# Kernel tuning notes

Hardware: AMD Instinct MI355X
Metric: run time of the kernel (lower is better)

The kernel has to match this reference:

```python
import jax, jax.numpy as jnp
import numpy as np

NEG_SLOPE = 0.2
EPS = 1e-16

N_NODES = 100000
N_EDGES = 1600000
IN_CH = 128
HEADS = 4
OUT_CH = 32


def setup_inputs() -> dict:
    key = jax.random.key(0)
    k1, k2, k3, k4, k5 = jax.random.split(key, 5)
    x = jax.random.normal(k1, (N_NODES, IN_CH), dtype=jnp.float32)
    edge_index = jax.random.randint(k2, (2, N_EDGES), 0, N_NODES, dtype=jnp.int64)
    glorot = (6.0 / (IN_CH + HEADS * OUT_CH)) ** 0.5
    W_l = jax.random.uniform(k3, (IN_CH, HEADS * OUT_CH), jnp.float32, -glorot, glorot)
    W_r = jax.random.uniform(k4, (IN_CH, HEADS * OUT_CH), jnp.float32, -glorot, glorot)
    ga = (6.0 / (OUT_CH + 1)) ** 0.5
    att = jax.random.uniform(k5, (HEADS, OUT_CH), jnp.float32, -ga, ga)
    bias = jnp.zeros((HEADS * OUT_CH,), dtype=jnp.float32)
    return {"x": x, "edge_index": edge_index, "W_l": W_l, "W_r": W_r, "att": att, "bias": bias}


def reference(x, edge_index, W_l, W_r, att, bias):
    # GATv2Conv forward (PyG semantics, concat=True, add_self_loops=False)
    N = x.shape[0]
    H, C = att.shape
    src, dst = edge_index[0], edge_index[1]

    x_l = (x @ W_l).reshape(N, H, C)  # source transform
    x_r = (x @ W_r).reshape(N, H, C)  # target transform

    # per-edge attention logits: e_ij = att . leaky_relu(x_l[j] + x_r[i])
    h = x_l[src] + x_r[dst]                      # [E, H, C]
    e = jnp.einsum('ehc,hc->eh', jax.nn.leaky_relu(h, NEG_SLOPE), att)  # [E, H]

    # segment softmax over edges grouped by destination node
    m = jax.ops.segment_max(e, dst, num_segments=N)      # [N, H]
    e_exp = jnp.exp(e - m[dst])                          # [E, H]
    denom = jax.ops.segment_sum(e_exp, dst, num_segments=N)  # [N, H]
    alpha = e_exp / (denom[dst] + EPS)                   # [E, H]

    # attention-weighted message aggregation
    msg = x_l[src] * alpha[:, :, None]                   # [E, H, C]
    out = jax.ops.segment_sum(msg, dst, num_segments=N)  # [N, H, C]
    return out.reshape(N, H * C) + bias
```

## Files before the change

### kernel.cpp

```cpp
#include <hip/hip_runtime.h>
#include <hip/hip_bf16.h>
#include <cstdint>
#include <cstddef>


#define NEG_SLOPE 0.2f
#define EPS_F 1e-16f
#define NRANGE 8
#define NCHUNK 64
#define SORT_B 1024
#define MAX_RSZ 12512

typedef __attribute__((ext_vector_type(8))) short bf16x8;
typedef __attribute__((ext_vector_type(4))) float f32x4;

static __device__ __forceinline__ unsigned f2bf(float f) {
    unsigned u = __float_as_uint(f);
    return (u + 0x7fffu + ((u >> 16) & 1u)) >> 16;
}
static __device__ __forceinline__ float bf2f(unsigned h) {
    return __uint_as_float(h << 16);
}

__global__ __launch_bounds__(SORT_B) void histW_k(const int* __restrict__ dst, int E, int N,
                                                  int rsz, int chunk_e,
                                                  unsigned* __restrict__ g,
                                                  const float* __restrict__ Wl,
                                                  const float* __restrict__ Wr,
                                                  unsigned short* __restrict__ Wtl,
                                                  unsigned short* __restrict__ Wtr) {
    if (blockIdx.x == NRANGE * NCHUNK) {
        for (int mat = 0; mat < 2; ++mat) {
            const float* W = mat ? Wr : Wl;
            unsigned short* Wt = mat ? Wtr : Wtl;
            for (int i = 0; i < 16; ++i) {
                int idx = (int)threadIdx.x + i * SORT_B;
                int k = idx >> 7, n = idx & 127;
                Wt[n * 128 + k] = (unsigned short)f2bf(W[idx]);
            }
        }
        return;
    }
    __shared__ unsigned lcnt[MAX_RSZ];
    const int r = blockIdx.x & (NRANGE - 1);
    const int c = blockIdx.x >> 3;
    const unsigned r_lo = (unsigned)(r * rsz);
    const int e0 = c * chunk_e;
    const int e1 = min(e0 + chunk_e, E);

    for (int i = threadIdx.x; i < rsz; i += SORT_B) lcnt[i] = 0u;
    __syncthreads();
    for (int e = e0 + (int)threadIdx.x; e < e1; e += SORT_B) {
        unsigned dd = (unsigned)dst[e] - r_lo;
        if (dd < (unsigned)rsz) atomicAdd(&lcnt[dd], 1u);
    }
    __syncthreads();
    unsigned* gc = g + (size_t)c * N + r_lo;
    int lim = min(rsz, N - (int)r_lo);
    for (int i = threadIdx.x; i < lim; i += SORT_B) gc[i] = lcnt[i];
}

#define LROW 136
__global__ __launch_bounds__(256) void mfma_gemm_k(const float* __restrict__ A,
                                                   const unsigned short* __restrict__ Wtl,
                                                   const unsigned short* __restrict__ Wtr,
                                                   unsigned short* __restrict__ xl,
                                                   unsigned short* __restrict__ xr,
                                                   int nrows) {
    __shared__ unsigned short As[64 * LROW];
    __shared__ unsigned short Ws[128 * LROW];
    const int tid = threadIdx.x;
    const int wave = tid >> 6, lane = tid & 63;
    const int quad = lane >> 4, m16 = lane & 15;
    const int row0 = blockIdx.x * 64;

#pragma unroll
    for (int i = 0; i < 8; ++i) {
        int idx = tid + i * 256;
        int r = idx >> 5, c4 = idx & 31;
        int gr = row0 + r;
        gr = gr < nrows ? gr : nrows - 1;
        float4 v = *(const float4*)(A + (size_t)gr * 128 + c4 * 4);
        ushort4 b;
        b.x = (unsigned short)f2bf(v.x);
        b.y = (unsigned short)f2bf(v.y);
        b.z = (unsigned short)f2bf(v.z);
        b.w = (unsigned short)f2bf(v.w);
        *(ushort4*)(&As[r * LROW + c4 * 4]) = b;
    }
#pragma unroll
    for (int i = 0; i < 8; ++i) {
        int idx = tid + i * 256;
        int n = idx >> 4, kq = idx & 15;
        *(uint4*)(&Ws[n * LROW + kq * 8]) = *(const uint4*)(Wtl + n * 128 + kq * 8);
    }
    __syncthreads();

    bf16x8 af[4];
#pragma unroll
    for (int ks = 0; ks < 4; ++ks)
        af[ks] = *(const bf16x8*)(&As[(wave * 16 + m16) * LROW + ks * 32 + quad * 8]);

    f32x4 acc[8];
#pragma unroll
    for (int ct = 0; ct < 8; ++ct) acc[ct] = (f32x4){0.f, 0.f, 0.f, 0.f};
#pragma unroll
    for (int ct = 0; ct < 8; ++ct)
#pragma unroll
        for (int ks = 0; ks < 4; ++ks) {
            bf16x8 bf = *(const bf16x8*)(&Ws[(ct * 16 + m16) * LROW + ks * 32 + quad * 8]);
            acc[ct] = __builtin_amdgcn_mfma_f32_16x16x32_bf16(af[ks], bf, acc[ct], 0, 0, 0);
        }
#pragma unroll
    for (int ct = 0; ct < 8; ++ct)
#pragma unroll
        for (int r = 0; r < 4; ++r) {
            int grow = row0 + wave * 16 + quad * 4 + r;
            if (grow < nrows) xl[(size_t)grow * 128 + ct * 16 + m16] = (unsigned short)f2bf(acc[ct][r]);
        }

    __syncthreads();
#pragma unroll
    for (int i = 0; i < 8; ++i) {
        int idx = tid + i * 256;
        int n = idx >> 4, kq = idx & 15;
        *(uint4*)(&Ws[n * LROW + kq * 8]) = *(const uint4*)(Wtr + n * 128 + kq * 8);
    }
    __syncthreads();

#pragma unroll
    for (int ct = 0; ct < 8; ++ct) acc[ct] = (f32x4){0.f, 0.f, 0.f, 0.f};
#pragma unroll
    for (int ct = 0; ct < 8; ++ct)
#pragma unroll
        for (int ks = 0; ks < 4; ++ks) {
            bf16x8 bf = *(const bf16x8*)(&Ws[(ct * 16 + m16) * LROW + ks * 32 + quad * 8]);
            acc[ct] = __builtin_amdgcn_mfma_f32_16x16x32_bf16(af[ks], bf, acc[ct], 0, 0, 0);
        }
#pragma unroll
    for (int ct = 0; ct < 8; ++ct)
#pragma unroll
        for (int r = 0; r < 4; ++r) {
            int grow = row0 + wave * 16 + quad * 4 + r;
            if (grow < nrows) xr[(size_t)grow * 128 + ct * 16 + m16] = (unsigned short)f2bf(acc[ct][r]);
        }
}

__global__ __launch_bounds__(256) void colsum_k(const unsigned* __restrict__ g, int N,
                                                int* __restrict__ cnt) {
    int d = blockIdx.x * 256 + threadIdx.x;
    if (d >= N) return;
    unsigned s = 0;
#pragma unroll
    for (int c = 0; c < NCHUNK; ++c) s += g[(size_t)c * N + d];
    cnt[d] = (int)s;
}

#define SCAN_B 256
__global__ __launch_bounds__(SCAN_B) void scanA_k(const int* __restrict__ cnt, int n,
                                                  int* __restrict__ row_start,
                                                  int* __restrict__ bsum) {
    const int tid = threadIdx.x, lane = tid & 63, wid = tid >> 6;
    const int g = blockIdx.x * SCAN_B + tid;
    int v = (g < n) ? cnt[g] : 0;
    int inc = v;
#pragma unroll
    for (int d = 1; d < 64; d <<= 1) {
        int t = __shfl_up(inc, d);
        if (lane >= d) inc += t;
    }
    __shared__ int wsum[SCAN_B / 64];
    if (lane == 63) wsum[wid] = inc;
    __syncthreads();
    int add = 0;
    for (int w = 0; w < wid; ++w) add += wsum[w];
    inc += add;
    if (g < n) row_start[g] = inc - v;
    if (tid == SCAN_B - 1) bsum[blockIdx.x] = inc;
}

__global__ __launch_bounds__(512) void scanB_k(int* __restrict__ bsum, int nb) {
    const int tid = threadIdx.x, lane = tid & 63, wid = tid >> 6;
    int v = (tid < nb) ? bsum[tid] : 0;
    int inc = v;
#pragma unroll
    for (int d = 1; d < 64; d <<= 1) {
        int t = __shfl_up(inc, d);
        if (lane >= d) inc += t;
    }
    __shared__ int wsum[8];
    if (lane == 63) wsum[wid] = inc;
    __syncthreads();
    int add = 0;
    for (int w = 0; w < wid; ++w) add += wsum[w];
    inc += add;
    if (tid < nb) bsum[tid] = inc - v;
}

__global__ __launch_bounds__(SCAN_B) void scanC_k(int* __restrict__ row_start,
                                                  const int* __restrict__ bsum,
                                                  int n, int E,
                                                  int* __restrict__ src_sorted) {
    const int g = blockIdx.x * SCAN_B + threadIdx.x;
    if (g < n) row_start[g] += bsum[blockIdx.x];
    if (g == 0) row_start[n] = E;
    if (blockIdx.x == 0 && threadIdx.x < 8) src_sorted[E + threadIdx.x] = 0;
}

__global__ __launch_bounds__(256) void cbase_k(const unsigned* __restrict__ g,
                                               const int* __restrict__ row_start, int N,
                                               unsigned* __restrict__ base) {
    int d = blockIdx.x * 256 + threadIdx.x;
    if (d >= N) return;
    unsigned run = (unsigned)row_start[d];
#pragma unroll
    for (int c = 0; c < NCHUNK; ++c) {
        base[(size_t)c * N + d] = run;
        run += g[(size_t)c * N + d];
    }
}

__global__ __launch_bounds__(SORT_B) void scat_k(const int* __restrict__ src,
                                                 const int* __restrict__ dst, int E, int N,
                                                 int rsz, int chunk_e,
                                                 const unsigned* __restrict__ base,
                                                 int* __restrict__ src_sorted) {
    __shared__ unsigned lcur[MAX_RSZ];
    const int r = blockIdx.x & (NRANGE - 1);
    const int c = blockIdx.x >> 3;
    const unsigned r_lo = (unsigned)(r * rsz);
    const int e0 = c * chunk_e;
    const int e1 = min(e0 + chunk_e, E);

    const unsigned* bc = base + (size_t)c * N + r_lo;
    int lim = min(rsz, N - (int)r_lo);
    for (int i = threadIdx.x; i < lim; i += SORT_B) lcur[i] = bc[i];
    __syncthreads();

    for (int e = e0 + (int)threadIdx.x; e < e1; e += SORT_B) {
        unsigned dd = (unsigned)dst[e] - r_lo;
        if (dd < (unsigned)rsz) {
            unsigned pos = atomicAdd(&lcur[dd], 1u);
            src_sorted[pos] = src[e];
        }
    }
}

__global__ __launch_bounds__(256) void agg_k(const unsigned* __restrict__ xlb,
                                             const unsigned* __restrict__ xrb,
                                             const float* __restrict__ att,
                                             const float* __restrict__ bias,
                                             const int* __restrict__ row_start,
                                             const int* __restrict__ src_sorted,
                                             int n, float* __restrict__ out) {
    const int wave = threadIdx.x >> 6;
    const int lane = threadIdx.x & 63;
    const int i = blockIdx.x * 4 + wave;
    if (i >= n) return;

    const int idx  = lane & 31;
    const int half = lane >> 5;

    uint2 xr2 = *(const uint2*)(xrb + (size_t)i * 64 + idx * 2);
    float xr0 = bf2f(xr2.x & 0xffffu), xr1 = bf2f(xr2.x >> 16);
    float xr2f = bf2f(xr2.y & 0xffffu), xr3 = bf2f(xr2.y >> 16);
    float4 at4 = *(const float4*)(att + idx * 4);

    const int k0 = row_start[i];
    const int k1 = row_start[i + 1];

    float l = 0.f, A0 = 0.f, A1 = 0.f, A2 = 0.f, A3 = 0.f;

    for (int k = k0; k < k1; k += 8) {
        const int kb = k + 4 * half;
        int s[4];
#pragma unroll
        for (int u = 0; u < 4; ++u) s[u] = src_sorted[kb + u];
        uint2 v[4];
#pragma unroll
        for (int u = 0; u < 4; ++u) v[u] = *(const uint2*)(xlb + (size_t)s[u] * 64 + idx * 2);
#pragma unroll
        for (int u = 0; u < 4; ++u) {
            float x0 = bf2f(v[u].x & 0xffffu), x1 = bf2f(v[u].x >> 16);
            float x2 = bf2f(v[u].y & 0xffffu), x3 = bf2f(v[u].y >> 16);
            float h0 = x0 + xr0, h1 = x1 + xr1, h2 = x2 + xr2f, h3 = x3 + xr3;
            h0 = fmaxf(h0, NEG_SLOPE * h0);
            h1 = fmaxf(h1, NEG_SLOPE * h1);
            h2 = fmaxf(h2, NEG_SLOPE * h2);
            h3 = fmaxf(h3, NEG_SLOPE * h3);
            float p = fmaf(at4.x, h0, at4.y * h1) + fmaf(at4.z, h2, at4.w * h3);
            p += __shfl_xor(p, 1);
            p += __shfl_xor(p, 2);
            p += __shfl_xor(p, 4);
            float w = (kb + u < k1) ? __expf(p) : 0.f;
            l += w;
            A0 = fmaf(w, x0, A0);
            A1 = fmaf(w, x1, A1);
            A2 = fmaf(w, x2, A2);
            A3 = fmaf(w, x3, A3);
        }
    }

    l  += __shfl_xor(l, 32);
    A0 += __shfl_xor(A0, 32);
    A1 += __shfl_xor(A1, 32);
    A2 += __shfl_xor(A2, 32);
    A3 += __shfl_xor(A3, 32);

    if (half == 0) {
        float inv = 1.f / (l + EPS_F);
        float4 b4 = *(const float4*)(bias + idx * 4);
        float4 o = {fmaf(A0, inv, b4.x), fmaf(A1, inv, b4.y),
                    fmaf(A2, inv, b4.z), fmaf(A3, inv, b4.w)};
        *(float4*)(out + (size_t)i * 128 + idx * 4) = o;
    }
}

extern "C" void kernel_launch(void* const* d_in, const int* in_sizes, int n_in,
                              void* d_out, int out_size, void* d_ws, size_t ws_size,
                              hipStream_t stream) {
    const float* x    = (const float*)d_in[0];
    const int*   ei   = (const int*)d_in[1];
    const float* W_l  = (const float*)d_in[2];
    const float* W_r  = (const float*)d_in[3];
    const float* att  = (const float*)d_in[4];
    const float* bias = (const float*)d_in[5];
    float* out = (float*)d_out;

    const int N = in_sizes[0] / 128;
    const int E = in_sizes[1] / 2;
    const int* src = ei;
    const int* dst = ei + E;

    char* ws = (char*)d_ws;
    size_t off = 0;
    auto alloc = [&](size_t bytes) {
        void* p = ws + off;
        off += (bytes + 15) & ~(size_t)15;
        return p;
    };
    unsigned* xlb     = (unsigned*)alloc((size_t)N * 64 * 4);
    unsigned* xrb     = (unsigned*)alloc((size_t)N * 64 * 4);
    unsigned* g       = (unsigned*)alloc((size_t)NCHUNK * N * 4);
    unsigned* base    = (unsigned*)alloc((size_t)NCHUNK * N * 4);
    int* cnt          = (int*)alloc((size_t)N * 4);
    int* row_start    = (int*)alloc((size_t)(N + 1) * 4);
    const int nsb = (N + SCAN_B - 1) / SCAN_B;
    int* bsum         = (int*)alloc((size_t)nsb * 4);
    int* src_sorted   = (int*)alloc((size_t)(E + 8) * 4);
    unsigned short* Wtl = (unsigned short*)alloc((size_t)128 * 128 * 2);
    unsigned short* Wtr = (unsigned short*)alloc((size_t)128 * 128 * 2);
    (void)ws_size;

    const int rsz = (N + NRANGE - 1) / NRANGE;
    const int chunk_e = (E + NCHUNK - 1) / NCHUNK;

    histW_k<<<NRANGE * NCHUNK + 1, SORT_B, 0, stream>>>(dst, E, N, rsz, chunk_e, g,
                                                        W_l, W_r, Wtl, Wtr);

    const int gB = (N + 63) / 64;
    mfma_gemm_k<<<gB, 256, 0, stream>>>(x, Wtl, Wtr,
                                        (unsigned short*)xlb, (unsigned short*)xrb, N);

    colsum_k<<<(N + 255) / 256, 256, 0, stream>>>(g, N, cnt);
    scanA_k<<<nsb, SCAN_B, 0, stream>>>(cnt, N, row_start, bsum);
    scanB_k<<<1, 512, 0, stream>>>(bsum, nsb);
    scanC_k<<<nsb, SCAN_B, 0, stream>>>(row_start, bsum, N, E, src_sorted);
    cbase_k<<<(N + 255) / 256, 256, 0, stream>>>(g, row_start, N, base);

    scat_k<<<NRANGE * NCHUNK, SORT_B, 0, stream>>>(src, dst, E, N, rsz, chunk_e,
                                                   base, src_sorted);

    agg_k<<<(N + 3) / 4, 256, 0, stream>>>(xlb, xrb, att, bias, row_start, src_sorted, N, out);
}
```

Before: 290.2 us.

## Fuse scan kernels, pack bf16 pairs in GEMM output, retune sort partitioning

Merges colsum into scanA and scanC into cbase, removing two launches and the cnt buffer. The GEMM now packs two bf16 column tiles into 32-bit stores with a permuted channel layout. att and bias are permuted to match, and att is prescaled by log2(e) so exp2f can be used. The sort partitioning changes from 8 ranges x 64 chunks to 16 x 32, which halves the LDS histogram size. The permuted layout needs a matching output scatter in agg_k, which adds index arithmetic and splits the float4 output store into two float2 stores.

```diff
diff --git a/kernel.cpp b/kernel.cpp
--- a/kernel.cpp
+++ b/kernel.cpp
@@ -6,10 +6,10 @@
 
 #define NEG_SLOPE 0.2f
 #define EPS_F 1e-16f
-#define NRANGE 8
-#define NCHUNK 64
+#define NRANGE 16
+#define NCHUNK 32
 #define SORT_B 1024
-#define MAX_RSZ 12512
+#define MAX_RSZ 6272
 
 typedef __attribute__((ext_vector_type(8))) short bf16x8;
 typedef __attribute__((ext_vector_type(4))) float f32x4;
@@ -17,9 +17,6 @@
 static __device__ __forceinline__ unsigned f2bf(float f) {
     unsigned u = __float_as_uint(f);
     return (u + 0x7fffu + ((u >> 16) & 1u)) >> 16;
-}
-static __device__ __forceinline__ float bf2f(unsigned h) {
-    return __uint_as_float(h << 16);
 }
 
 __global__ __launch_bounds__(SORT_B) void histW_k(const int* __restrict__ dst, int E, int N,
@@ -28,7 +25,11 @@
                                                   const float* __restrict__ Wl,
                                                   const float* __restrict__ Wr,
                                                   unsigned short* __restrict__ Wtl,
-                                                  unsigned short* __restrict__ Wtr) {
+                                                  unsigned short* __restrict__ Wtr,
+                                                  const float* __restrict__ att,
+                                                  const float* __restrict__ bias,
+                                                  float* __restrict__ attP,
+                                                  float* __restrict__ biasP) {
     if (blockIdx.x == NRANGE * NCHUNK) {
         for (int mat = 0; mat < 2; ++mat) {
             const float* W = mat ? Wr : Wl;
@@ -39,11 +40,19 @@
                 Wt[n * 128 + k] = (unsigned short)f2bf(W[idx]);
             }
         }
+        if (threadIdx.x < 128) {
+            int j = threadIdx.x;
+            int h = j >> 5, r = j & 31;
+            int m16 = r >> 1, b = r & 1;
+            int col = (2 * h + b) * 16 + m16;
+            attP[j]  = att[col] * 1.44269504088896f;
+            biasP[j] = bias[col];
+        }
         return;
     }
     __shared__ unsigned lcnt[MAX_RSZ];
     const int r = blockIdx.x & (NRANGE - 1);
-    const int c = blockIdx.x >> 3;
+    const int c = blockIdx.x >> 4;
     const unsigned r_lo = (unsigned)(r * rsz);
     const int e0 = c * chunk_e;
     const int e1 = min(e0 + chunk_e, E);
@@ -64,8 +73,8 @@
 __global__ __launch_bounds__(256) void mfma_gemm_k(const float* __restrict__ A,
                                                    const unsigned short* __restrict__ Wtl,
                                                    const unsigned short* __restrict__ Wtr,
-                                                   unsigned short* __restrict__ xl,
-                                                   unsigned short* __restrict__ xr,
+                                                   unsigned* __restrict__ xl32,
+                                                   unsigned* __restrict__ xr32,
                                                    int nrows) {
     __shared__ unsigned short As[64 * LROW];
     __shared__ unsigned short Ws[128 * LROW];
@@ -112,12 +121,14 @@
             acc[ct] = __builtin_amdgcn_mfma_f32_16x16x32_bf16(af[ks], bf, acc[ct], 0, 0, 0);
         }
 #pragma unroll
-    for (int ct = 0; ct < 8; ++ct)
-#pragma unroll
-        for (int r = 0; r < 4; ++r) {
-            int grow = row0 + wave * 16 + quad * 4 + r;
-            if (grow < nrows) xl[(size_t)grow * 128 + ct * 16 + m16] = (unsigned short)f2bf(acc[ct][r]);
-        }
+    for (int r = 0; r < 4; ++r) {
+        int grow = row0 + wave * 16 + quad * 4 + r;
+        if (grow < nrows)
+#pragma unroll
+            for (int h = 0; h < 4; ++h)
+                xl32[(size_t)grow * 64 + h * 16 + m16] =
+                    f2bf(acc[2 * h][r]) | (f2bf(acc[2 * h + 1][r]) << 16);
+    }
 
     __syncthreads();
 #pragma unroll
@@ -138,36 +149,34 @@
             acc[ct] = __builtin_amdgcn_mfma_f32_16x16x32_bf16(af[ks], bf, acc[ct], 0, 0, 0);
         }
 #pragma unroll
-    for (int ct = 0; ct < 8; ++ct)
-#pragma unroll
-        for (int r = 0; r < 4; ++r) {
-            int grow = row0 + wave * 16 + quad * 4 + r;
-            if (grow < nrows) xr[(size_t)grow * 128 + ct * 16 + m16] = (unsigned short)f2bf(acc[ct][r]);
-        }
-}
-
-__global__ __launch_bounds__(256) void colsum_k(const unsigned* __restrict__ g, int N,
-                                                int* __restrict__ cnt) {
-    int d = blockIdx.x * 256 + threadIdx.x;
-    if (d >= N) return;
-    unsigned s = 0;
-#pragma unroll
-    for (int c = 0; c < NCHUNK; ++c) s += g[(size_t)c * N + d];
-    cnt[d] = (int)s;
+    for (int r = 0; r < 4; ++r) {
+        int grow = row0 + wave * 16 + quad * 4 + r;
+        if (grow < nrows)
+#pragma unroll
+            for (int h = 0; h < 4; ++h)
+                xr32[(size_t)grow * 64 + h * 16 + m16] =
+                    f2bf(acc[2 * h][r]) | (f2bf(acc[2 * h + 1][r]) << 16);
+    }
 }
 
 #define SCAN_B 256
-__global__ __launch_bounds__(SCAN_B) void scanA_k(const int* __restrict__ cnt, int n,
+__global__ __launch_bounds__(SCAN_B) void scanA_k(const unsigned* __restrict__ g, int n,
                                                   int* __restrict__ row_start,
                                                   int* __restrict__ bsum) {
     const int tid = threadIdx.x, lane = tid & 63, wid = tid >> 6;
-    const int g = blockIdx.x * SCAN_B + tid;
-    int v = (g < n) ? cnt[g] : 0;
+    const int d = blockIdx.x * SCAN_B + tid;
+    int v = 0;
+    if (d < n) {
+        unsigned s = 0;
+#pragma unroll
+        for (int c = 0; c < NCHUNK; ++c) s += g[(size_t)c * n + d];
+        v = (int)s;
+    }
     int inc = v;
 #pragma unroll
-    for (int d = 1; d < 64; d <<= 1) {
-        int t = __shfl_up(inc, d);
-        if (lane >= d) inc += t;
+    for (int dd = 1; dd < 64; dd <<= 1) {
+        int t = __shfl_up(inc, dd);
+        if (lane >= dd) inc += t;
     }
     __shared__ int wsum[SCAN_B / 64];
     if (lane == 63) wsum[wid] = inc;
@@ -175,7 +184,7 @@
     int add = 0;
     for (int w = 0; w < wid; ++w) add += wsum[w];
     inc += add;
-    if (g < n) row_start[g] = inc - v;
+    if (d < n) row_start[d] = inc - v;
     if (tid == SCAN_B - 1) bsum[blockIdx.x] = inc;
 }
 
@@ -197,27 +206,24 @@
     if (tid < nb) bsum[tid] = inc - v;
 }
 
-__global__ __launch_bounds__(SCAN_B) void scanC_k(int* __restrict__ row_start,
+__global__ __launch_bounds__(SCAN_B) void cbase_k(const unsigned* __restrict__ g,
                                                   const int* __restrict__ bsum,
-                                                  int n, int E,
+                                                  int* __restrict__ row_start, int N, int E,
+                                                  unsigned* __restrict__ base,
                                                   int* __restrict__ src_sorted) {
-    const int g = blockIdx.x * SCAN_B + threadIdx.x;
-    if (g < n) row_start[g] += bsum[blockIdx.x];
-    if (g == 0) row_start[n] = E;
+    const int d = blockIdx.x * SCAN_B + threadIdx.x;
+    if (d < N) {
+        int rs = row_start[d] + bsum[blockIdx.x];
+        row_start[d] = rs;
+        unsigned run = (unsigned)rs;
+#pragma unroll
+        for (int c = 0; c < NCHUNK; ++c) {
+            base[(size_t)c * N + d] = run;
+            run += g[(size_t)c * N + d];
+        }
+    }
+    if (d == 0) row_start[N] = E;
     if (blockIdx.x == 0 && threadIdx.x < 8) src_sorted[E + threadIdx.x] = 0;
-}
-
-__global__ __launch_bounds__(256) void cbase_k(const unsigned* __restrict__ g,
-                                               const int* __restrict__ row_start, int N,
-                                               unsigned* __restrict__ base) {
-    int d = blockIdx.x * 256 + threadIdx.x;
-    if (d >= N) return;
-    unsigned run = (unsigned)row_start[d];
-#pragma unroll
-    for (int c = 0; c < NCHUNK; ++c) {
-        base[(size_t)c * N + d] = run;
-        run += g[(size_t)c * N + d];
-    }
 }
 
 __global__ __launch_bounds__(SORT_B) void scat_k(const int* __restrict__ src,
@@ -227,7 +233,7 @@
                                                  int* __restrict__ src_sorted) {
     __shared__ unsigned lcur[MAX_RSZ];
     const int r = blockIdx.x & (NRANGE - 1);
-    const int c = blockIdx.x >> 3;
+    const int c = blockIdx.x >> 4;
     const unsigned r_lo = (unsigned)(r * rsz);
     const int e0 = c * chunk_e;
     const int e1 = min(e0 + chunk_e, E);
@@ -248,8 +254,8 @@
 
 __global__ __launch_bounds__(256) void agg_k(const unsigned* __restrict__ xlb,
                                              const unsigned* __restrict__ xrb,
-                                             const float* __restrict__ att,
-                                             const float* __restrict__ bias,
+                                             const float* __restrict__ attP,
+                                             const float* __restrict__ biasP,
                                              const int* __restrict__ row_start,
                                              const int* __restrict__ src_sorted,
                                              int n, float* __restrict__ out) {
@@ -262,14 +268,18 @@
     const int half = lane >> 5;
 
     uint2 xr2 = *(const uint2*)(xrb + (size_t)i * 64 + idx * 2);
-    float xr0 = bf2f(xr2.x & 0xffffu), xr1 = bf2f(xr2.x >> 16);
-    float xr2f = bf2f(xr2.y & 0xffffu), xr3 = bf2f(xr2.y >> 16);
-    float4 at4 = *(const float4*)(att + idx * 4);
+    const float xr0 = __uint_as_float(xr2.x << 16);
+    const float xr1 = __uint_as_float(xr2.x & 0xffff0000u);
+    const float xr2f = __uint_as_float(xr2.y << 16);
+    const float xr3 = __uint_as_float(xr2.y & 0xffff0000u);
+    const float4 at4 = *(const float4*)(attP + idx * 4);
 
     const int k0 = row_start[i];
     const int k1 = row_start[i + 1];
 
     float l = 0.f, A0 = 0.f, A1 = 0.f, A2 = 0.f, A3 = 0.f;
+    const char* xlbc = (const char*)xlb;
+    const unsigned lane_off = (unsigned)(idx << 3);
 
     for (int k = k0; k < k1; k += 8) {
         const int kb = k + 4 * half;
@@ -278,11 +288,16 @@
         for (int u = 0; u < 4; ++u) s[u] = src_sorted[kb + u];
         uint2 v[4];
 #pragma unroll
-        for (int u = 0; u < 4; ++u) v[u] = *(const uint2*)(xlb + (size_t)s[u] * 64 + idx * 2);
-#pragma unroll
         for (int u = 0; u < 4; ++u) {
-            float x0 = bf2f(v[u].x & 0xffffu), x1 = bf2f(v[u].x >> 16);
-            float x2 = bf2f(v[u].y & 0xffffu), x3 = bf2f(v[u].y >> 16);
+            unsigned off = ((unsigned)s[u] << 8) + lane_off;
+            v[u] = *(const uint2*)(xlbc + off);
+        }
+#pragma unroll
+        for (int u = 0; u < 4; ++u) {
+            float x0 = __uint_as_float(v[u].x << 16);
+            float x1 = __uint_as_float(v[u].x & 0xffff0000u);
+            float x2 = __uint_as_float(v[u].y << 16);
+            float x3 = __uint_as_float(v[u].y & 0xffff0000u);
             float h0 = x0 + xr0, h1 = x1 + xr1, h2 = x2 + xr2f, h3 = x3 + xr3;
             h0 = fmaxf(h0, NEG_SLOPE * h0);
             h1 = fmaxf(h1, NEG_SLOPE * h1);
@@ -292,7 +307,7 @@
             p += __shfl_xor(p, 1);
             p += __shfl_xor(p, 2);
             p += __shfl_xor(p, 4);
-            float w = (kb + u < k1) ? __expf(p) : 0.f;
+            float w = (kb + u < k1) ? exp2f(p) : 0.f;
             l += w;
             A0 = fmaf(w, x0, A0);
             A1 = fmaf(w, x1, A1);
@@ -309,10 +324,13 @@
 
     if (half == 0) {
         float inv = 1.f / (l + EPS_F);
-        float4 b4 = *(const float4*)(bias + idx * 4);
-        float4 o = {fmaf(A0, inv, b4.x), fmaf(A1, inv, b4.y),
-                    fmaf(A2, inv, b4.z), fmaf(A3, inv, b4.w)};
-        *(float4*)(out + (size_t)i * 128 + idx * 4) = o;
+        float4 b4 = *(const float4*)(biasP + idx * 4);
+        const int h = idx >> 3;
+        const int c0 = 32 * h + 2 * (idx & 7);
+        float2 oA = {fmaf(A0, inv, b4.x), fmaf(A2, inv, b4.z)};
+        float2 oB = {fmaf(A1, inv, b4.y), fmaf(A3, inv, b4.w)};
+        *(float2*)(out + (size_t)i * 128 + c0) = oA;
+        *(float2*)(out + (size_t)i * 128 + c0 + 16) = oB;
     }
 }
 
@@ -343,33 +361,33 @@
     unsigned* xrb     = (unsigned*)alloc((size_t)N * 64 * 4);
     unsigned* g       = (unsigned*)alloc((size_t)NCHUNK * N * 4);
     unsigned* base    = (unsigned*)alloc((size_t)NCHUNK * N * 4);
-    int* cnt          = (int*)alloc((size_t)N * 4);
     int* row_start    = (int*)alloc((size_t)(N + 1) * 4);
     const int nsb = (N + SCAN_B - 1) / SCAN_B;
     int* bsum         = (int*)alloc((size_t)nsb * 4);
     int* src_sorted   = (int*)alloc((size_t)(E + 8) * 4);
     unsigned short* Wtl = (unsigned short*)alloc((size_t)128 * 128 * 2);
     unsigned short* Wtr = (unsigned short*)alloc((size_t)128 * 128 * 2);
+    float* attP       = (float*)alloc(128 * 4);
+    float* biasP      = (float*)alloc(128 * 4);
     (void)ws_size;
 
     const int rsz = (N + NRANGE - 1) / NRANGE;
     const int chunk_e = (E + NCHUNK - 1) / NCHUNK;
 
     histW_k<<<NRANGE * NCHUNK + 1, SORT_B, 0, stream>>>(dst, E, N, rsz, chunk_e, g,
-                                                        W_l, W_r, Wtl, Wtr);
+                                                        W_l, W_r, Wtl, Wtr,
+                                                        att, bias, attP, biasP);
 
     const int gB = (N + 63) / 64;
-    mfma_gemm_k<<<gB, 256, 0, stream>>>(x, Wtl, Wtr,
-                                        (unsigned short*)xlb, (unsigned short*)xrb, N);
-
-    colsum_k<<<(N + 255) / 256, 256, 0, stream>>>(g, N, cnt);
-    scanA_k<<<nsb, SCAN_B, 0, stream>>>(cnt, N, row_start, bsum);
+    mfma_gemm_k<<<gB, 256, 0, stream>>>(x, Wtl, Wtr, xlb, xrb, N);
+
+    scanA_k<<<nsb, SCAN_B, 0, stream>>>(g, N, row_start, bsum);
     scanB_k<<<1, 512, 0, stream>>>(bsum, nsb);
-    scanC_k<<<nsb, SCAN_B, 0, stream>>>(row_start, bsum, N, E, src_sorted);
-    cbase_k<<<(N + 255) / 256, 256, 0, stream>>>(g, row_start, N, base);
+    cbase_k<<<nsb, SCAN_B, 0, stream>>>(g, bsum, row_start, N, E, base, src_sorted);
 
     scat_k<<<NRANGE * NCHUNK, SORT_B, 0, stream>>>(src, dst, E, N, rsz, chunk_e,
                                                    base, src_sorted);
 
-    agg_k<<<(N + 3) / 4, 256, 0, stream>>>(xlb, xrb, att, bias, row_start, src_sorted, N, out);
-}
+    agg_k<<<(N + 3) / 4, 256, 0, stream>>>(xlb, xrb, attP, biasP,
+                                           row_start, src_sorted, N, out);
+}
```

New measurement: 303.6 us. +4.6%, slower.
